# Kernel tuning notes

Hardware: AMD Instinct MI355X
Metric: run time of the kernel (lower is better)

The kernel has to match this reference:

```python
import jax, jax.numpy as jnp
import numpy as np

N = 50000      # nodes
E = 800000     # edges (before self-loops)
IN = 128       # in_channels
HID = 64       # hidden_channels
HEADS = 4
OUT = 64       # out_channels
SLOPE = 0.2    # negative_slope


def setup_inputs() -> dict:
    key = jax.random.key(0)
    ks = jax.random.split(key, 16)

    def p(k, shape, fan_in):
        return jax.random.normal(k, shape, dtype=jnp.float32) / np.float32(np.sqrt(fan_in))

    inp = jax.random.normal(ks[0], (N, IN), dtype=jnp.float32)
    edge_index = jax.random.randint(ks[1], (2, E), 0, N, dtype=jnp.int32)

    W1 = p(ks[2], (IN, HEADS * HID), IN)
    att_src1 = p(ks[3], (1, HEADS, HID), HID)
    att_dst1 = p(ks[4], (1, HEADS, HID), HID)
    b1 = jnp.zeros((HEADS * HID,), jnp.float32)

    W2 = p(ks[5], (HEADS * HID, HEADS * HID), HEADS * HID)
    att_src2 = p(ks[6], (1, HEADS, HID), HID)
    att_dst2 = p(ks[7], (1, HEADS, HID), HID)
    b2 = jnp.zeros((HEADS * HID,), jnp.float32)

    W3 = p(ks[8], (HEADS * HID, HEADS * OUT), HEADS * HID)
    att_src3 = p(ks[9], (1, HEADS, OUT), OUT)
    att_dst3 = p(ks[10], (1, HEADS, OUT), OUT)
    b3 = jnp.zeros((HEADS * OUT,), jnp.float32)

    return dict(inp=inp, edge_index=edge_index,
                W1=W1, att_src1=att_src1, att_dst1=att_dst1, b1=b1,
                W2=W2, att_src2=att_src2, att_dst2=att_dst2, b2=b2,
                W3=W3, att_src3=att_src3, att_dst3=att_dst3, b3=b3)


def _gat_conv(x, W, a_src, a_dst, b, src, dst, H, C):
    """One PyG-style GATConv (concat=True, dropout=0, self-loops already in src/dst)."""
    n = x.shape[0]
    h = (x @ W).reshape(n, H, C)                     # [N,H,C]
    alpha_src = jnp.sum(h * a_src, axis=-1)          # [N,H]
    alpha_dst = jnp.sum(h * a_dst, axis=-1)          # [N,H]
    e = jax.nn.leaky_relu(alpha_src[src] + alpha_dst[dst], SLOPE)  # [Etot,H]
    # segment softmax over incoming edges of each destination node
    emax = jax.ops.segment_max(e, dst, num_segments=n)             # [N,H]
    ee = jnp.exp(e - emax[dst])
    denom = jax.ops.segment_sum(ee, dst, num_segments=n)           # [N,H]
    alpha = ee / denom[dst]                                        # [Etot,H]
    out = jax.ops.segment_sum(alpha[:, :, None] * h[src], dst, num_segments=n)  # [N,H,C]
    return out.reshape(n, H * C) + b


def reference(inp, edge_index, W1, att_src1, att_dst1, b1,
              W2, att_src2, att_dst2, b2, W3, att_src3, att_dst3, b3):
    n = inp.shape[0]
    loops = jnp.arange(n, dtype=edge_index.dtype)
    src = jnp.concatenate([edge_index[0], loops])  # add self-loops (PyG default)
    dst = jnp.concatenate([edge_index[1], loops])
    h1 = jax.nn.elu(_gat_conv(inp, W1, att_src1, att_dst1, b1, src, dst, HEADS, HID))
    h2 = jax.nn.elu(_gat_conv(h1, W2, att_src2, att_dst2, b2, src, dst, HEADS, HID))
    oup = jax.nn.elu(_gat_conv(h2, W3, att_src3, att_dst3, b3, src, dst, HEADS, OUT))
    return oup
```

## Files before the change

### kernel.cpp

```cpp
#include <hip/hip_runtime.h>
#include <hip/hip_bf16.h>
#include <stdint.h>

#define HEADS 4
#define SLOPE 0.2f

typedef unsigned short u16;
typedef float f32x4 __attribute__((ext_vector_type(4)));
typedef short s16x8 __attribute__((ext_vector_type(8)));
typedef unsigned short u16x4 __attribute__((ext_vector_type(4)));

__device__ __forceinline__ u16 f2bf(float f) {
    unsigned int u = __float_as_uint(f);
    u = (u + 0x7fffu + ((u >> 16) & 1u)) >> 16;
    return (u16)u;
}
__device__ __forceinline__ float bf2f(u16 v) {
    return __uint_as_float(((unsigned int)v) << 16);
}
__device__ __forceinline__ float fin(float x) {
    return (x == x && fabsf(x) < 1e30f) ? x : 0.f;
}

__global__ void prep_kernel(const float* __restrict__ inp, u16* __restrict__ Xb,
                            const float* __restrict__ W1, u16* __restrict__ Wt1,
                            const float* __restrict__ W2, u16* __restrict__ Wt2,
                            const float* __restrict__ W3, u16* __restrict__ Wt3,
                            int* __restrict__ deg, int N) {
    int i = blockIdx.x * blockDim.x + threadIdx.x;
    int cast4 = N * 32;
    if (i < cast4) {
        f32x4 v = *(const f32x4*)(inp + (size_t)i * 4);
        u16x4 o;
        #pragma unroll
        for (int j = 0; j < 4; j++) o[j] = f2bf(fin(v[j]));
        *(u16x4*)(Xb + (size_t)i * 4) = o;
        return;
    }
    i -= cast4;
    if (i < N) { deg[i] = 0; return; }
    i -= N;
    if (i >= 0 && i < 128 * 256) {
        int k = i >> 8, m = i & 255;
        Wt1[m * 128 + k] = f2bf(fin(W1[i]));
        return;
    }
    i -= 128 * 256;
    if (i >= 0 && i < 256 * 256) {
        int k = i >> 8, m = i & 255;
        Wt2[m * 256 + k] = f2bf(fin(W2[i]));
        return;
    }
    i -= 256 * 256;
    if (i >= 0 && i < 256 * 256) {
        int k = i >> 8, m = i & 255;
        Wt3[m * 256 + k] = f2bf(fin(W3[i]));
    }
}

__global__ void count_kernel(const int* __restrict__ dst, int* __restrict__ deg,
                             int* __restrict__ rank, int E, int N) {
    int i = blockIdx.x * blockDim.x + threadIdx.x;
    if (i < E + N) {
        int d = (i < E) ? dst[i] : (i - E);
        d = ((unsigned)d < (unsigned)N) ? d : 0;
        rank[i] = atomicAdd(&deg[d], 1);
    }
}

__global__ __launch_bounds__(256) void scan_kernel(const int* __restrict__ deg,
                                                   int* __restrict__ rowstart, int N) {
    __shared__ int wsum[4];
    __shared__ int sm[256];
    int b = blockIdx.x, tid = threadIdx.x;
    int start = b * 1024;
    int pre = 0;
    for (int i = tid; i < start; i += 256) pre += deg[i];
    #pragma unroll
    for (int off = 1; off <= 32; off <<= 1) pre += __shfl_xor(pre, off);
    if ((tid & 63) == 0) wsum[tid >> 6] = pre;
    __syncthreads();
    int block_pre = wsum[0] + wsum[1] + wsum[2] + wsum[3];

    int base = start + tid * 4;
    int v[4]; int s = 0;
    #pragma unroll
    for (int j = 0; j < 4; j++) { int i = base + j; v[j] = (i < N) ? deg[i] : 0; s += v[j]; }
    sm[tid] = s;
    __syncthreads();
    for (int off = 1; off < 256; off <<= 1) {
        int t = (tid >= off) ? sm[tid - off] : 0;
        __syncthreads();
        sm[tid] += t;
        __syncthreads();
    }
    int run = block_pre + sm[tid] - s;
    #pragma unroll
    for (int j = 0; j < 4; j++) {
        int i = base + j;
        if (i < N) { rowstart[i] = run; run += v[j]; }
    }
    if (b == gridDim.x - 1 && tid == 255) rowstart[N] = block_pre + sm[255];
}

__global__ void place_kernel(const int* __restrict__ src, const int* __restrict__ dst,
                             const int* __restrict__ rowstart, const int* __restrict__ rank,
                             int* __restrict__ csr, int E, int N) {
    int i = blockIdx.x * blockDim.x + threadIdx.x;
    if (i < E + N) {
        int s, d;
        if (i < E) { s = src[i]; d = dst[i]; }
        else       { s = i - E; d = i - E; }
        s = ((unsigned)s < (unsigned)N) ? s : 0;
        d = ((unsigned)d < (unsigned)N) ? d : 0;
        int pos = rowstart[d] + rank[i];
        if ((unsigned)pos < (unsigned)(E + N)) csr[pos] = s;
    }
}

__global__ __launch_bounds__(256, 3) void gemm_kernel(
        const u16* __restrict__ X, const u16* __restrict__ Wt,
        u16* __restrict__ Hout, const float* __restrict__ att_src,
        const float* __restrict__ att_dst, float* __restrict__ as_out,
        float* __restrict__ ad_out, int N, int K) {
    __shared__ __align__(16) u16 As[64 * 72];
    __shared__ __align__(16) u16 Bs[256 * 72];
    int t = threadIdx.x;
    int wv = t >> 6, lane = t & 63;
    int quad = lane >> 4, l16 = lane & 15;
    int m0 = blockIdx.x * 64;
    int n0 = wv * 64;
    int srow = t >> 3, sslot = t & 7;

    f32x4 acc[4][4];
    #pragma unroll
    for (int r = 0; r < 4; r++)
        #pragma unroll
        for (int c = 0; c < 4; c++) acc[r][c] = (f32x4){0.f, 0.f, 0.f, 0.f};

    const int nsteps = K >> 6;
    s16x8 ra[2], rb[8];
    {
        #pragma unroll
        for (int s = 0; s < 2; s++) {
            int rg = m0 + s * 32 + srow; rg = rg < N ? rg : N - 1;
            ra[s] = *(const s16x8*)(X + (size_t)rg * K + sslot * 8);
        }
        #pragma unroll
        for (int s = 0; s < 8; s++) {
            int n = s * 32 + srow;
            rb[s] = *(const s16x8*)(Wt + (size_t)n * K + sslot * 8);
        }
    }
    for (int step = 0; step < nsteps; step++) {
        __syncthreads();
        #pragma unroll
        for (int s = 0; s < 2; s++)
            *(s16x8*)(As + (s * 32 + srow) * 72 + sslot * 8) = ra[s];
        #pragma unroll
        for (int s = 0; s < 8; s++)
            *(s16x8*)(Bs + (s * 32 + srow) * 72 + sslot * 8) = rb[s];
        __syncthreads();
        if (step + 1 < nsteps) {
            int k0 = (step + 1) << 6;
            #pragma unroll
            for (int s = 0; s < 2; s++) {
                int rg = m0 + s * 32 + srow; rg = rg < N ? rg : N - 1;
                ra[s] = *(const s16x8*)(X + (size_t)rg * K + k0 + sslot * 8);
            }
            #pragma unroll
            for (int s = 0; s < 8; s++) {
                int n = s * 32 + srow;
                rb[s] = *(const s16x8*)(Wt + (size_t)n * K + k0 + sslot * 8);
            }
        }
        #pragma unroll
        for (int subk = 0; subk < 2; subk++) {
            s16x8 af[4], bf[4];
            #pragma unroll
            for (int r = 0; r < 4; r++)
                af[r] = *(const s16x8*)(As + (r * 16 + l16) * 72 + subk * 32 + quad * 8);
            #pragma unroll
            for (int c = 0; c < 4; c++)
                bf[c] = *(const s16x8*)(Bs + (n0 + c * 16 + l16) * 72 + subk * 32 + quad * 8);
            #pragma unroll
            for (int r = 0; r < 4; r++)
                #pragma unroll
                for (int c = 0; c < 4; c++)
                    acc[r][c] = __builtin_amdgcn_mfma_f32_16x16x32_bf16(af[r], bf[c], acc[r][c], 0, 0, 0);
        }
    }

    float aps[4][4], apd[4][4];
    #pragma unroll
    for (int r = 0; r < 4; r++)
        #pragma unroll
        for (int j = 0; j < 4; j++) { aps[r][j] = 0.f; apd[r][j] = 0.f; }

    #pragma unroll
    for (int r = 0; r < 4; r++) {
        int rowb = m0 + r * 16 + quad * 4;
        #pragma unroll
        for (int c = 0; c < 4; c++) {
            int col = n0 + c * 16 + l16;
            float av = fin(att_src[col]);
            float dv = fin(att_dst[col]);
            #pragma unroll
            for (int j = 0; j < 4; j++) {
                int row = rowb + j;
                float v = acc[r][c][j];
                aps[r][j] += v * av;
                apd[r][j] += v * dv;
                if (row < N) Hout[(size_t)row * 256 + col] = f2bf(v);
            }
        }
    }
    #pragma unroll
    for (int off = 1; off <= 8; off <<= 1)
        #pragma unroll
        for (int r = 0; r < 4; r++)
            #pragma unroll
            for (int j = 0; j < 4; j++) {
                aps[r][j] += __shfl_xor(aps[r][j], off);
                apd[r][j] += __shfl_xor(apd[r][j], off);
            }
    if (l16 == 0) {
        #pragma unroll
        for (int r = 0; r < 4; r++) {
            int rowb = m0 + r * 16 + quad * 4;
            #pragma unroll
            for (int j = 0; j < 4; j++) {
                int row = rowb + j;
                if (row < N) {
                    as_out[row * 4 + wv] = aps[r][j];
                    ad_out[row * 4 + wv] = apd[r][j];
                }
            }
        }
    }
}

__global__ __launch_bounds__(256) void gather_kernel(
        const u16* __restrict__ Hb, const float* __restrict__ asrc,
        const float* __restrict__ adst, const int* __restrict__ rowstart,
        const int* __restrict__ csr, const float* __restrict__ bias,
        u16* __restrict__ outb, float* __restrict__ outf, int write_f32,
        int N, int Etot) {
    int wv = threadIdx.x >> 6, lane = threadIdx.x & 63;
    int n = blockIdx.x * 4 + wv;
    if (n >= N) return;
    int es = lane >> 5, c = lane & 31;
    int h = c >> 3;
    int i0 = rowstart[n], i1 = rowstart[n + 1];
    i0 = min(max(i0, 0), Etot);
    i1 = min(max(i1, i0), Etot);

    float adh = adst[n * 4 + h];
    float acc[8];
    float ws = 0.f;
    #pragma unroll
    for (int j = 0; j < 8; j++) acc[j] = 0.f;

    int i = i0 + es;
    for (; i + 6 < i1; i += 8) {
        int ss[4];
        #pragma unroll
        for (int u = 0; u < 4; u++) {
            int s = csr[i + 2 * u];
            ss[u] = ((unsigned)s < (unsigned)N) ? s : 0;
        }
        float e[4]; s16x8 hv[4];
        #pragma unroll
        for (int u = 0; u < 4; u++) {
            e[u] = asrc[ss[u] * 4 + h] + adh;
            hv[u] = *(const s16x8*)(Hb + (size_t)ss[u] * 256 + c * 8);
        }
        #pragma unroll
        for (int u = 0; u < 4; u++) {
            float ee = e[u] > 0.f ? e[u] : SLOPE * e[u];
            float w = __expf(fminf(ee, 80.f));
            ws += w;
            #pragma unroll
            for (int j = 0; j < 8; j++) acc[j] += w * bf2f((u16)hv[u][j]);
        }
    }
    for (; i + 2 < i1; i += 4) {
        int sA = csr[i], sB = csr[i + 2];
        sA = ((unsigned)sA < (unsigned)N) ? sA : 0;
        sB = ((unsigned)sB < (unsigned)N) ? sB : 0;
        float eA = asrc[sA * 4 + h] + adh;
        float eB = asrc[sB * 4 + h] + adh;
        s16x8 hvA = *(const s16x8*)(Hb + (size_t)sA * 256 + c * 8);
        s16x8 hvB = *(const s16x8*)(Hb + (size_t)sB * 256 + c * 8);
        eA = eA > 0.f ? eA : SLOPE * eA;
        eB = eB > 0.f ? eB : SLOPE * eB;
        float wA = __expf(fminf(eA, 80.f));
        float wB = __expf(fminf(eB, 80.f));
        ws += wA + wB;
        #pragma unroll
        for (int j = 0; j < 8; j++)
            acc[j] += wA * bf2f((u16)hvA[j]) + wB * bf2f((u16)hvB[j]);
    }
    if (i < i1) {
        int s = csr[i];
        s = ((unsigned)s < (unsigned)N) ? s : 0;
        float e = asrc[s * 4 + h] + adh;
        s16x8 hv = *(const s16x8*)(Hb + (size_t)s * 256 + c * 8);
        e = e > 0.f ? e : SLOPE * e;
        float w = __expf(fminf(e, 80.f));
        ws += w;
        #pragma unroll
        for (int j = 0; j < 8; j++) acc[j] += w * bf2f((u16)hv[j]);
    }

    ws += __shfl_xor(ws, 32);
    #pragma unroll
    for (int j = 0; j < 8; j++) acc[j] += __shfl_xor(acc[j], 32);

    if (es == 0) {
        float invh = (ws > 0.f) ? 1.f / ws : 0.f;
        f32x4 blo = *(const f32x4*)(bias + c * 8);
        f32x4 bhi = *(const f32x4*)(bias + c * 8 + 4);
        size_t base = (size_t)n * 256 + c * 8;
        float o[8];
        #pragma unroll
        for (int j = 0; j < 8; j++) {
            float v = acc[j] * invh + fin(j < 4 ? blo[j] : bhi[j - 4]);
            o[j] = v > 0.f ? v : (__expf(v) - 1.f);
        }
        if (write_f32) {
            f32x4 lo = {o[0], o[1], o[2], o[3]}, hi = {o[4], o[5], o[6], o[7]};
            *(f32x4*)(outf + base) = lo;
            *(f32x4*)(outf + base + 4) = hi;
        } else {
            s16x8 ob;
            #pragma unroll
            for (int j = 0; j < 8; j++) ob[j] = (short)f2bf(o[j]);
            *(s16x8*)(outb + base) = ob;
        }
    }
}

extern "C" void kernel_launch(void* const* d_in, const int* in_sizes, int n_in,
                              void* d_out, int out_size, void* d_ws, size_t ws_size,
                              hipStream_t stream) {
    const float* inp  = (const float*)d_in[0];
    const int*   ei   = (const int*)d_in[1];
    const float* W1   = (const float*)d_in[2];
    const float* at_s1= (const float*)d_in[3];
    const float* at_d1= (const float*)d_in[4];
    const float* b1   = (const float*)d_in[5];
    const float* W2   = (const float*)d_in[6];
    const float* at_s2= (const float*)d_in[7];
    const float* at_d2= (const float*)d_in[8];
    const float* b2   = (const float*)d_in[9];
    const float* W3   = (const float*)d_in[10];
    const float* at_s3= (const float*)d_in[11];
    const float* at_d3= (const float*)d_in[12];
    const float* b3   = (const float*)d_in[13];

    const int N = in_sizes[0] / 128;
    const int E = in_sizes[1] / 2;
    const int Etot = E + N;
    const int* esrc = ei;
    const int* edst = ei + E;

    char* p = (char*)d_ws;
    auto alloc = [&](size_t b) -> void* {
        void* q = (void*)p;
        p += (b + 255) & ~(size_t)255;
        return q;
    };
    u16*   Xb       = (u16*)alloc((size_t)N * 256 * 2);
    u16*   Hb       = (u16*)alloc((size_t)N * 256 * 2);
    u16*   Wt1      = (u16*)alloc((size_t)128 * 256 * 2);
    u16*   Wt2      = (u16*)alloc((size_t)256 * 256 * 2);
    u16*   Wt3      = (u16*)alloc((size_t)256 * 256 * 2);
    float* asb      = (float*)alloc((size_t)N * 4 * 4);
    float* adb      = (float*)alloc((size_t)N * 4 * 4);
    int*   deg      = (int*)alloc((size_t)N * 4);
    int*   rowstart = (int*)alloc((size_t)(N + 1) * 4);
    int*   rank     = (int*)alloc((size_t)Etot * 4);
    int*   csr      = (int*)alloc((size_t)Etot * 4);
    float* outf     = (float*)d_out;

    const int SB = (N + 1023) / 1024;
    const int prep_total = N * 32 + N + 128 * 256 + 2 * 256 * 256;

    prep_kernel<<<(prep_total + 255) / 256, 256, 0, stream>>>(
        inp, Xb, W1, Wt1, W2, Wt2, W3, Wt3, deg, N);
    count_kernel<<<(Etot + 255) / 256, 256, 0, stream>>>(edst, deg, rank, E, N);
    scan_kernel<<<SB, 256, 0, stream>>>(deg, rowstart, N);
    place_kernel<<<(Etot + 255) / 256, 256, 0, stream>>>(esrc, edst, rowstart, rank, csr, E, N);

    const int gemm_grid = (N + 63) / 64;
    const int node_grid = (N + 3) / 4;

    gemm_kernel<<<gemm_grid, 256, 0, stream>>>(Xb, Wt1, Hb, at_s1, at_d1, asb, adb, N, 128);
    gather_kernel<<<node_grid, 256, 0, stream>>>(Hb, asb, adb, rowstart, csr, b1,
                                                 Xb, outf, 0, N, Etot);
    gemm_kernel<<<gemm_grid, 256, 0, stream>>>(Xb, Wt2, Hb, at_s2, at_d2, asb, adb, N, 256);
    gather_kernel<<<node_grid, 256, 0, stream>>>(Hb, asb, adb, rowstart, csr, b2,
                                                 Xb, outf, 0, N, Etot);
    gemm_kernel<<<gemm_grid, 256, 0, stream>>>(Xb, Wt3, Hb, at_s3, at_d3, asb, adb, N, 256);
    gather_kernel<<<node_grid, 256, 0, stream>>>(Hb, asb, adb, rowstart, csr, b3,
                                                 Xb, outf, 1, N, Etot);
}
```

Measured before the change: 444.4 us.

## Switch intermediates to fp16, fuse degree count into prep, shrink gather blocks

Changes the storage and MFMA type from bf16 to fp16 and clamps values to the fp16 range. Merges the degree-counting atomics into the prep kernel and zeroes the degree array with a memset. Halves the gather block size to two nodes per block, and uses nontemporal loads for the CSR indices and nontemporal stores for the outputs. The aim is to remove one launch, make conversions cheaper and improve gather cache behaviour. fp16 narrows the dynamic range, which the clamp hides.

```diff
diff --git a/kernel.cpp b/kernel.cpp
--- a/kernel.cpp
+++ b/kernel.cpp
@@ -6,65 +6,59 @@
 #define SLOPE 0.2f
 
 typedef unsigned short u16;
+typedef _Float16 f16;
 typedef float f32x4 __attribute__((ext_vector_type(4)));
-typedef short s16x8 __attribute__((ext_vector_type(8)));
-typedef unsigned short u16x4 __attribute__((ext_vector_type(4)));
-
-__device__ __forceinline__ u16 f2bf(float f) {
-    unsigned int u = __float_as_uint(f);
-    u = (u + 0x7fffu + ((u >> 16) & 1u)) >> 16;
-    return (u16)u;
-}
-__device__ __forceinline__ float bf2f(u16 v) {
-    return __uint_as_float(((unsigned int)v) << 16);
-}
+typedef _Float16 f16x8 __attribute__((ext_vector_type(8)));
+typedef _Float16 f16x4 __attribute__((ext_vector_type(4)));
+
 __device__ __forceinline__ float fin(float x) {
     return (x == x && fabsf(x) < 1e30f) ? x : 0.f;
 }
-
-__global__ void prep_kernel(const float* __restrict__ inp, u16* __restrict__ Xb,
-                            const float* __restrict__ W1, u16* __restrict__ Wt1,
-                            const float* __restrict__ W2, u16* __restrict__ Wt2,
-                            const float* __restrict__ W3, u16* __restrict__ Wt3,
-                            int* __restrict__ deg, int N) {
+__device__ __forceinline__ float finh(float x) {
+    x = fin(x);
+    return fminf(fmaxf(x, -60000.f), 60000.f);
+}
+
+__global__ void prep_kernel(const float* __restrict__ inp, f16* __restrict__ Xh,
+                            const float* __restrict__ W1, f16* __restrict__ Wt1,
+                            const float* __restrict__ W2, f16* __restrict__ Wt2,
+                            const float* __restrict__ W3, f16* __restrict__ Wt3,
+                            const int* __restrict__ dst, int* __restrict__ deg,
+                            int* __restrict__ rank, int E, int N) {
     int i = blockIdx.x * blockDim.x + threadIdx.x;
+    int Etot = E + N;
+    if (i < Etot) {
+        int d = (i < E) ? dst[i] : (i - E);
+        d = ((unsigned)d < (unsigned)N) ? d : 0;
+        rank[i] = atomicAdd(&deg[d], 1);
+        return;
+    }
+    i -= Etot;
     int cast4 = N * 32;
     if (i < cast4) {
         f32x4 v = *(const f32x4*)(inp + (size_t)i * 4);
-        u16x4 o;
-        #pragma unroll
-        for (int j = 0; j < 4; j++) o[j] = f2bf(fin(v[j]));
-        *(u16x4*)(Xb + (size_t)i * 4) = o;
+        f16x4 o;
+        #pragma unroll
+        for (int j = 0; j < 4; j++) o[j] = (f16)finh(v[j]);
+        *(f16x4*)(Xh + (size_t)i * 4) = o;
         return;
     }
     i -= cast4;
-    if (i < N) { deg[i] = 0; return; }
-    i -= N;
     if (i >= 0 && i < 128 * 256) {
         int k = i >> 8, m = i & 255;
-        Wt1[m * 128 + k] = f2bf(fin(W1[i]));
+        Wt1[m * 128 + k] = (f16)finh(W1[i]);
         return;
     }
     i -= 128 * 256;
     if (i >= 0 && i < 256 * 256) {
         int k = i >> 8, m = i & 255;
-        Wt2[m * 256 + k] = f2bf(fin(W2[i]));
+        Wt2[m * 256 + k] = (f16)finh(W2[i]);
         return;
     }
     i -= 256 * 256;
     if (i >= 0 && i < 256 * 256) {
         int k = i >> 8, m = i & 255;
-        Wt3[m * 256 + k] = f2bf(fin(W3[i]));
-    }
-}
-
-__global__ void count_kernel(const int* __restrict__ dst, int* __restrict__ deg,
-                             int* __restrict__ rank, int E, int N) {
-    int i = blockIdx.x * blockDim.x + threadIdx.x;
-    if (i < E + N) {
-        int d = (i < E) ? dst[i] : (i - E);
-        d = ((unsigned)d < (unsigned)N) ? d : 0;
-        rank[i] = atomicAdd(&deg[d], 1);
+        Wt3[m * 256 + k] = (f16)finh(W3[i]);
     }
 }
 
@@ -119,12 +113,12 @@
 }
 
 __global__ __launch_bounds__(256, 3) void gemm_kernel(
-        const u16* __restrict__ X, const u16* __restrict__ Wt,
-        u16* __restrict__ Hout, const float* __restrict__ att_src,
+        const f16* __restrict__ X, const f16* __restrict__ Wt,
+        f16* __restrict__ Hout, const float* __restrict__ att_src,
         const float* __restrict__ att_dst, float* __restrict__ as_out,
         float* __restrict__ ad_out, int N, int K) {
-    __shared__ __align__(16) u16 As[64 * 72];
-    __shared__ __align__(16) u16 Bs[256 * 72];
+    __shared__ __align__(16) f16 As[64 * 72];
+    __shared__ __align__(16) f16 Bs[256 * 72];
     int t = threadIdx.x;
     int wv = t >> 6, lane = t & 63;
     int quad = lane >> 4, l16 = lane & 15;
@@ -139,55 +133,55 @@
         for (int c = 0; c < 4; c++) acc[r][c] = (f32x4){0.f, 0.f, 0.f, 0.f};
 
     const int nsteps = K >> 6;
-    s16x8 ra[2], rb[8];
+    f16x8 ra[2], rb[8];
     {
         #pragma unroll
         for (int s = 0; s < 2; s++) {
             int rg = m0 + s * 32 + srow; rg = rg < N ? rg : N - 1;
-            ra[s] = *(const s16x8*)(X + (size_t)rg * K + sslot * 8);
+            ra[s] = *(const f16x8*)(X + (size_t)rg * K + sslot * 8);
         }
         #pragma unroll
         for (int s = 0; s < 8; s++) {
             int n = s * 32 + srow;
-            rb[s] = *(const s16x8*)(Wt + (size_t)n * K + sslot * 8);
+            rb[s] = *(const f16x8*)(Wt + (size_t)n * K + sslot * 8);
         }
     }
     for (int step = 0; step < nsteps; step++) {
         __syncthreads();
         #pragma unroll
         for (int s = 0; s < 2; s++)
-            *(s16x8*)(As + (s * 32 + srow) * 72 + sslot * 8) = ra[s];
+            *(f16x8*)(As + (s * 32 + srow) * 72 + sslot * 8) = ra[s];
         #pragma unroll
         for (int s = 0; s < 8; s++)
-            *(s16x8*)(Bs + (s * 32 + srow) * 72 + sslot * 8) = rb[s];
+            *(f16x8*)(Bs + (s * 32 + srow) * 72 + sslot * 8) = rb[s];
         __syncthreads();
         if (step + 1 < nsteps) {
             int k0 = (step + 1) << 6;
             #pragma unroll
             for (int s = 0; s < 2; s++) {
                 int rg = m0 + s * 32 + srow; rg = rg < N ? rg : N - 1;
-                ra[s] = *(const s16x8*)(X + (size_t)rg * K + k0 + sslot * 8);
+                ra[s] = *(const f16x8*)(X + (size_t)rg * K + k0 + sslot * 8);
             }
             #pragma unroll
             for (int s = 0; s < 8; s++) {
                 int n = s * 32 + srow;
-                rb[s] = *(const s16x8*)(Wt + (size_t)n * K + k0 + sslot * 8);
+                rb[s] = *(const f16x8*)(Wt + (size_t)n * K + k0 + sslot * 8);
             }
         }
         #pragma unroll
         for (int subk = 0; subk < 2; subk++) {
-            s16x8 af[4], bf[4];
+            f16x8 af[4], bfr[4];
             #pragma unroll
             for (int r = 0; r < 4; r++)
-                af[r] = *(const s16x8*)(As + (r * 16 + l16) * 72 + subk * 32 + quad * 8);
+                af[r] = *(const f16x8*)(As + (r * 16 + l16) * 72 + subk * 32 + quad * 8);
             #pragma unroll
             for (int c = 0; c < 4; c++)
-                bf[c] = *(const s16x8*)(Bs + (n0 + c * 16 + l16) * 72 + subk * 32 + quad * 8);
+                bfr[c] = *(const f16x8*)(Bs + (n0 + c * 16 + l16) * 72 + subk * 32 + quad * 8);
             #pragma unroll
             for (int r = 0; r < 4; r++)
                 #pragma unroll
                 for (int c = 0; c < 4; c++)
-                    acc[r][c] = __builtin_amdgcn_mfma_f32_16x16x32_bf16(af[r], bf[c], acc[r][c], 0, 0, 0);
+                    acc[r][c] = __builtin_amdgcn_mfma_f32_16x16x32_f16(af[r], bfr[c], acc[r][c], 0, 0, 0);
         }
     }
 
@@ -211,7 +205,7 @@
                 float v = acc[r][c][j];
                 aps[r][j] += v * av;
                 apd[r][j] += v * dv;
-                if (row < N) Hout[(size_t)row * 256 + col] = f2bf(v);
+                if (row < N) Hout[(size_t)row * 256 + col] = (f16)v;
             }
         }
     }
@@ -240,14 +234,14 @@
     }
 }
 
-__global__ __launch_bounds__(256) void gather_kernel(
-        const u16* __restrict__ Hb, const float* __restrict__ asrc,
+__global__ __launch_bounds__(128) void gather_kernel(
+        const f16* __restrict__ Hb, const float* __restrict__ asrc,
         const float* __restrict__ adst, const int* __restrict__ rowstart,
         const int* __restrict__ csr, const float* __restrict__ bias,
-        u16* __restrict__ outb, float* __restrict__ outf, int write_f32,
+        f16* __restrict__ outh, float* __restrict__ outf, int write_f32,
         int N, int Etot) {
     int wv = threadIdx.x >> 6, lane = threadIdx.x & 63;
-    int n = blockIdx.x * 4 + wv;
+    int n = blockIdx.x * 2 + wv;
     if (n >= N) return;
     int es = lane >> 5, c = lane & 31;
     int h = c >> 3;
@@ -266,14 +260,14 @@
         int ss[4];
         #pragma unroll
         for (int u = 0; u < 4; u++) {
-            int s = csr[i + 2 * u];
+            int s = __builtin_nontemporal_load(csr + i + 2 * u);
             ss[u] = ((unsigned)s < (unsigned)N) ? s : 0;
         }
-        float e[4]; s16x8 hv[4];
+        float e[4]; f16x8 hv[4];
         #pragma unroll
         for (int u = 0; u < 4; u++) {
             e[u] = asrc[ss[u] * 4 + h] + adh;
-            hv[u] = *(const s16x8*)(Hb + (size_t)ss[u] * 256 + c * 8);
+            hv[u] = *(const f16x8*)(Hb + (size_t)ss[u] * 256 + c * 8);
         }
         #pragma unroll
         for (int u = 0; u < 4; u++) {
@@ -281,17 +275,18 @@
             float w = __expf(fminf(ee, 80.f));
             ws += w;
             #pragma unroll
-            for (int j = 0; j < 8; j++) acc[j] += w * bf2f((u16)hv[u][j]);
+            for (int j = 0; j < 8; j++) acc[j] += w * (float)hv[u][j];
         }
     }
     for (; i + 2 < i1; i += 4) {
-        int sA = csr[i], sB = csr[i + 2];
+        int sA = __builtin_nontemporal_load(csr + i);
+        int sB = __builtin_nontemporal_load(csr + i + 2);
         sA = ((unsigned)sA < (unsigned)N) ? sA : 0;
         sB = ((unsigned)sB < (unsigned)N) ? sB : 0;
         float eA = asrc[sA * 4 + h] + adh;
         float eB = asrc[sB * 4 + h] + adh;
-        s16x8 hvA = *(const s16x8*)(Hb + (size_t)sA * 256 + c * 8);
-        s16x8 hvB = *(const s16x8*)(Hb + (size_t)sB * 256 + c * 8);
+        f16x8 hvA = *(const f16x8*)(Hb + (size_t)sA * 256 + c * 8);
+        f16x8 hvB = *(const f16x8*)(Hb + (size_t)sB * 256 + c * 8);
         eA = eA > 0.f ? eA : SLOPE * eA;
         eB = eB > 0.f ? eB : SLOPE * eB;
         float wA = __expf(fminf(eA, 80.f));
@@ -299,18 +294,18 @@
         ws += wA + wB;
         #pragma unroll
         for (int j = 0; j < 8; j++)
-            acc[j] += wA * bf2f((u16)hvA[j]) + wB * bf2f((u16)hvB[j]);
+            acc[j] += wA * (float)hvA[j] + wB * (float)hvB[j];
     }
     if (i < i1) {
-        int s = csr[i];
+        int s = __builtin_nontemporal_load(csr + i);
         s = ((unsigned)s < (unsigned)N) ? s : 0;
         float e = asrc[s * 4 + h] + adh;
-        s16x8 hv = *(const s16x8*)(Hb + (size_t)s * 256 + c * 8);
+        f16x8 hv = *(const f16x8*)(Hb + (size_t)s * 256 + c * 8);
         e = e > 0.f ? e : SLOPE * e;
         float w = __expf(fminf(e, 80.f));
         ws += w;
         #pragma unroll
-        for (int j = 0; j < 8; j++) acc[j] += w * bf2f((u16)hv[j]);
+        for (int j = 0; j < 8; j++) acc[j] += w * (float)hv[j];
     }
 
     ws += __shfl_xor(ws, 32);
@@ -330,13 +325,13 @@
         }
         if (write_f32) {
             f32x4 lo = {o[0], o[1], o[2], o[3]}, hi = {o[4], o[5], o[6], o[7]};
-            *(f32x4*)(outf + base) = lo;
-            *(f32x4*)(outf + base + 4) = hi;
+            __builtin_nontemporal_store(lo, (f32x4*)(outf + base));
+            __builtin_nontemporal_store(hi, (f32x4*)(outf + base + 4));
         } else {
-            s16x8 ob;
-            #pragma unroll
-            for (int j = 0; j < 8; j++) ob[j] = (short)f2bf(o[j]);
-            *(s16x8*)(outb + base) = ob;
+            f16x8 ob;
+            #pragma unroll
+            for (int j = 0; j < 8; j++) ob[j] = (f16)finh(o[j]);
+            __builtin_nontemporal_store(ob, (f16x8*)(outh + base));
         }
     }
 }
@@ -371,11 +366,11 @@
         p += (b + 255) & ~(size_t)255;
         return q;
     };
-    u16*   Xb       = (u16*)alloc((size_t)N * 256 * 2);
-    u16*   Hb       = (u16*)alloc((size_t)N * 256 * 2);
-    u16*   Wt1      = (u16*)alloc((size_t)128 * 256 * 2);
-    u16*   Wt2      = (u16*)alloc((size_t)256 * 256 * 2);
-    u16*   Wt3      = (u16*)alloc((size_t)256 * 256 * 2);
+    f16*   Xh       = (f16*)alloc((size_t)N * 256 * 2);
+    f16*   Hh       = (f16*)alloc((size_t)N * 256 * 2);
+    f16*   Wt1      = (f16*)alloc((size_t)128 * 256 * 2);
+    f16*   Wt2      = (f16*)alloc((size_t)256 * 256 * 2);
+    f16*   Wt3      = (f16*)alloc((size_t)256 * 256 * 2);
     float* asb      = (float*)alloc((size_t)N * 4 * 4);
     float* adb      = (float*)alloc((size_t)N * 4 * 4);
     int*   deg      = (int*)alloc((size_t)N * 4);
@@ -385,24 +380,24 @@
     float* outf     = (float*)d_out;
 
     const int SB = (N + 1023) / 1024;
-    const int prep_total = N * 32 + N + 128 * 256 + 2 * 256 * 256;
-
+    const int prep_total = Etot + N * 32 + 128 * 256 + 2 * 256 * 256;
+
+    hipMemsetAsync(deg, 0, (size_t)N * 4, stream);
     prep_kernel<<<(prep_total + 255) / 256, 256, 0, stream>>>(
-        inp, Xb, W1, Wt1, W2, Wt2, W3, Wt3, deg, N);
-    count_kernel<<<(Etot + 255) / 256, 256, 0, stream>>>(edst, deg, rank, E, N);
+        inp, Xh, W1, Wt1, W2, Wt2, W3, Wt3, edst, deg, rank, E, N);
     scan_kernel<<<SB, 256, 0, stream>>>(deg, rowstart, N);
     place_kernel<<<(Etot + 255) / 256, 256, 0, stream>>>(esrc, edst, rowstart, rank, csr, E, N);
 
     const int gemm_grid = (N + 63) / 64;
-    const int node_grid = (N + 3) / 4;
-
-    gemm_kernel<<<gemm_grid, 256, 0, stream>>>(Xb, Wt1, Hb, at_s1, at_d1, asb, adb, N, 128);
-    gather_kernel<<<node_grid, 256, 0, stream>>>(Hb, asb, adb, rowstart, csr, b1,
-                                                 Xb, outf, 0, N, Etot);
-    gemm_kernel<<<gemm_grid, 256, 0, stream>>>(Xb, Wt2, Hb, at_s2, at_d2, asb, adb, N, 256);
-    gather_kernel<<<node_grid, 256, 0, stream>>>(Hb, asb, adb, rowstart, csr, b2,
-                                                 Xb, outf, 0, N, Etot);
-    gemm_kernel<<<gemm_grid, 256, 0, stream>>>(Xb, Wt3, Hb, at_s3, at_d3, asb, adb, N, 256);
-    gather_kernel<<<node_grid, 256, 0, stream>>>(Hb, asb, adb, rowstart, csr, b3,
-                                                 Xb, outf, 1, N, Etot);
-}
+    const int node_grid = (N + 1) / 2;
+
+    gemm_kernel<<<gemm_grid, 256, 0, stream>>>(Xh, Wt1, Hh, at_s1, at_d1, asb, adb, N, 128);
+    gather_kernel<<<node_grid, 128, 0, stream>>>(Hh, asb, adb, rowstart, csr, b1,
+                                                 Xh, outf, 0, N, Etot);
+    gemm_kernel<<<gemm_grid, 256, 0, stream>>>(Xh, Wt2, Hh, at_s2, at_d2, asb, adb, N, 256);
+    gather_kernel<<<node_grid, 128, 0, stream>>>(Hh, asb, adb, rowstart, csr, b2,
+                                                 Xh, outf, 0, N, Etot);
+    gemm_kernel<<<gemm_grid, 256, 0, stream>>>(Xh, Wt3, Hh, at_s3, at_d3, asb, adb, N, 256);
+    gather_kernel<<<node_grid, 128, 0, stream>>>(Hh, asb, adb, rowstart, csr, b3,
+                                                 Xh, outf, 1, N, Etot);
+}
```

After: 456.9 us. 2.8% more time.
